# Performance work log

Hardware: AMD Instinct MI355X
Metric: run time of the kernel (lower is better)

Reference implementation:

```python
import jax, jax.numpy as jnp
import numpy as np

N_NODES = 100000
N_EDGES = 1600000
IN_FEATS = 16
H_FEAT = 128
NUM_CLASSES = 4
N_HIDDEN_LAYERS = 19  # layers 2..20 (128->128)
NEG_SLOPE = 0.01      # torch nn.LeakyReLU default


def setup_inputs() -> dict:
    key = jax.random.key(0)
    ks = jax.random.split(key, 10)
    node_feat = jax.random.normal(ks[0], (N_NODES, IN_FEATS), dtype=jnp.float32)
    edge_weight = jax.random.uniform(ks[1], (N_EDGES,), dtype=jnp.float32)
    src = jax.random.randint(ks[2], (N_EDGES,), 0, N_NODES, dtype=jnp.int32)
    dst = jax.random.randint(ks[3], (N_EDGES,), 0, N_NODES, dtype=jnp.int32)
    # Glorot-ish init for GraphConv weights, zero biases (DGL default)
    W1 = jax.random.normal(ks[4], (IN_FEATS, H_FEAT), dtype=jnp.float32) * (1.0 / np.sqrt(IN_FEATS))
    b1 = jnp.zeros((H_FEAT,), dtype=jnp.float32)
    W_stack = jax.random.normal(ks[5], (N_HIDDEN_LAYERS, H_FEAT, H_FEAT), dtype=jnp.float32) * (1.0 / np.sqrt(H_FEAT))
    b_stack = jnp.zeros((N_HIDDEN_LAYERS, H_FEAT), dtype=jnp.float32)
    fc_W = jax.random.normal(ks[6], (H_FEAT, NUM_CLASSES), dtype=jnp.float32) * (1.0 / np.sqrt(H_FEAT))
    fc_b = jnp.zeros((NUM_CLASSES,), dtype=jnp.float32)
    return {"node_feat": node_feat, "edge_weight": edge_weight, "src": src, "dst": dst,
            "W1": W1, "b1": b1, "W_stack": W_stack, "b_stack": b_stack,
            "fc_W": fc_W, "fc_b": fc_b}


def _degree_norms(src, dst, n_nodes, dtype):
    ones = jnp.ones(src.shape, dtype=dtype)
    out_deg = jax.ops.segment_sum(ones, src, num_segments=n_nodes)
    in_deg = jax.ops.segment_sum(ones, dst, num_segments=n_nodes)
    # DGL clamps degrees to min 1 for norm='both'
    inv_sqrt_out = jax.lax.rsqrt(jnp.maximum(out_deg, 1.0))
    inv_sqrt_in = jax.lax.rsqrt(jnp.maximum(in_deg, 1.0))
    return inv_sqrt_out, inv_sqrt_in


def _graph_conv(h, W, b, src, dst, ew, inv_sqrt_out, inv_sqrt_in, n_nodes):
    # DGL GraphConv norm='both' with edge_weight: u_mul_e message, sum at dst
    hs = h * inv_sqrt_out[:, None]                     # [N, F] src-side norm
    m = hs[src] * ew[:, None]                          # [E, F] edge messages
    agg = jax.ops.segment_sum(m, dst, num_segments=n_nodes)  # [N, F]
    agg = agg * inv_sqrt_in[:, None]                   # dst-side norm
    return agg @ W + b


def reference(node_feat, edge_weight, src, dst, W1, b1, W_stack, b_stack, fc_W, fc_b):
    n_nodes = node_feat.shape[0]
    iso, isi = _degree_norms(src, dst, n_nodes, node_feat.dtype)
    leaky = lambda x: jnp.where(x >= 0, x, NEG_SLOPE * x)

    h = leaky(_graph_conv(node_feat, W1, b1, src, dst, edge_weight, iso, isi, n_nodes))

    def body(h, wb):
        W, b = wb
        h = leaky(_graph_conv(h, W, b, src, dst, edge_weight, iso, isi, n_nodes))
        return h, None

    h, _ = jax.lax.scan(body, h, (W_stack, b_stack))
    return h @ fc_W + fc_b
```

## Files before the change

kernel.cpp:

```cpp
#include <hip/hip_runtime.h>

#define NN 100000
#define NE 1600000
#define HF 128
#define INF 16
#define NLAYERS 19

static inline int idiv(int a, int b) { return (a + b - 1) / b; }

__device__ __forceinline__ float leaky(float v) { return (v >= 0.f) ? v : 0.01f * v; }


__global__ __launch_bounds__(256) void k_deg1(const int* __restrict__ idx, int* __restrict__ deg, int e) {
  int i = (blockIdx.x * 256 + threadIdx.x) * 4;
  if (i + 4 <= e) {
    int4 v = *reinterpret_cast<const int4*>(idx + i);
    atomicAdd(&deg[v.x], 1);
    atomicAdd(&deg[v.y], 1);
    atomicAdd(&deg[v.z], 1);
    atomicAdd(&deg[v.w], 1);
  } else {
    for (; i < e; ++i) atomicAdd(&deg[idx[i]], 1);
  }
}

__global__ __launch_bounds__(256) void k_norms(const int* __restrict__ dout, const int* __restrict__ din,
                                               float* __restrict__ iso, float* __restrict__ isi, int n) {
  int i = blockIdx.x * 256 + threadIdx.x;
  if (i < n) {
    iso[i] = rsqrtf((float)(dout[i] > 1 ? dout[i] : 1));
    isi[i] = rsqrtf((float)(din[i] > 1 ? din[i] : 1));
  }
}

__global__ __launch_bounds__(1024) void k_scan(const int* __restrict__ cnt, int* __restrict__ rp, int n) {
  __shared__ int wsum[16];
  const int tid = threadIdx.x;
  const int lane = tid & 63;
  const int wid = tid >> 6;
  int carry = 0;
  for (int base = 0; base < n; base += 1024) {
    int i = base + tid;
    int v = (i < n) ? cnt[i] : 0;
    int x = v;
#pragma unroll
    for (int off = 1; off < 64; off <<= 1) {
      int t = __shfl_up(x, off, 64);
      if (lane >= off) x += t;
    }
    if (lane == 63) wsum[wid] = x;
    __syncthreads();
    if (wid == 0) {
      int s = (lane < 16) ? wsum[lane] : 0;
#pragma unroll
      for (int off = 1; off < 16; off <<= 1) {
        int t = __shfl_up(s, off, 64);
        if (lane >= off) s += t;
      }
      if (lane < 16) wsum[lane] = s;
    }
    __syncthreads();
    int woff = (wid > 0) ? wsum[wid - 1] : 0;
    if (i < n) rp[i] = carry + woff + x - v;
    carry += wsum[15];
    __syncthreads();
  }
  if (tid == 0) rp[n] = carry;
}

__global__ __launch_bounds__(256) void k_build(const int* __restrict__ src, const int* __restrict__ dst,
                                               const float* __restrict__ ew, const float* __restrict__ iso,
                                               const float* __restrict__ isi, const int* __restrict__ rp,
                                               int* __restrict__ cursor, int2* __restrict__ cv, int e) {
  int i = blockIdx.x * 256 + threadIdx.x;
  if (i < e) {
    int s = src[i], d = dst[i];
    int pos = rp[d] + atomicAdd(&cursor[d], 1);
    float v = ew[i] * iso[s] * isi[d];
    cv[pos] = make_int2(s, __float_as_int(v));
  }
}


__global__ __launch_bounds__(256) void k_spmm16(const float* __restrict__ x, const int* __restrict__ rp,
                                                const int2* __restrict__ cv, float* __restrict__ agg16, int n) {
  int t = blockIdx.x * 256 + threadIdx.x;
  int node = t >> 4, f = t & 15;
  if (node >= n) return;
  int e = rp[node], end = rp[node + 1];
  float a = 0.f;
  for (; e + 4 <= end; e += 4) {
    int2 q0 = cv[e], q1 = cv[e + 1], q2 = cv[e + 2], q3 = cv[e + 3];
    float x0 = x[(size_t)q0.x * INF + f];
    float x1 = x[(size_t)q1.x * INF + f];
    float x2 = x[(size_t)q2.x * INF + f];
    float x3 = x[(size_t)q3.x * INF + f];
    a = fmaf(__int_as_float(q0.y), x0, a);
    a = fmaf(__int_as_float(q1.y), x1, a);
    a = fmaf(__int_as_float(q2.y), x2, a);
    a = fmaf(__int_as_float(q3.y), x3, a);
  }
  for (; e < end; ++e) {
    int2 q = cv[e];
    a = fmaf(__int_as_float(q.y), x[(size_t)q.x * INF + f], a);
  }
  agg16[(size_t)node * INF + f] = a;
}

__global__ __launch_bounds__(256) void k_gemm16(const float* __restrict__ agg16, const float* __restrict__ W1,
                                                const float* __restrict__ b1, float* __restrict__ h, int n) {
  __shared__ float W1s[INF * HF];
  int tid = threadIdx.x;
  {
    float4* d4 = reinterpret_cast<float4*>(W1s);
    const float4* s4 = reinterpret_cast<const float4*>(W1);
    d4[tid] = s4[tid];
    d4[tid + 256] = s4[tid + 256];
  }
  __syncthreads();
  int t = blockIdx.x * 256 + tid;
  int node = t >> 7, c = t & 127;
  if (node >= n) return;
  const float* ar = agg16 + (size_t)node * INF;
  float4 a0 = *reinterpret_cast<const float4*>(ar);
  float4 a1 = *reinterpret_cast<const float4*>(ar + 4);
  float4 a2 = *reinterpret_cast<const float4*>(ar + 8);
  float4 a3 = *reinterpret_cast<const float4*>(ar + 12);
  float av[16] = {a0.x, a0.y, a0.z, a0.w, a1.x, a1.y, a1.z, a1.w,
                  a2.x, a2.y, a2.z, a2.w, a3.x, a3.y, a3.z, a3.w};
  float a = b1[c];
#pragma unroll
  for (int f = 0; f < INF; ++f) a = fmaf(av[f], W1s[f * HF + c], a);
  h[(size_t)t] = leaky(a);
}


__global__ __launch_bounds__(256) void k_spmm(const float* __restrict__ h, const int* __restrict__ rp,
                                              const int2* __restrict__ cv, float* __restrict__ agg, int n) {
  const int lane = threadIdx.x & 63;
  const int node = __builtin_amdgcn_readfirstlane(blockIdx.x * 4 + (threadIdx.x >> 6));
  if (node >= n) return;
  const int beg = rp[node], end = rp[node + 1];
  const size_t fo = (size_t)(lane << 1);
  float ax = 0.f, ay = 0.f;
  int e = beg;
  for (; e + 8 <= end; e += 8) {
    int2 q0 = cv[e + 0], q1 = cv[e + 1], q2 = cv[e + 2], q3 = cv[e + 3];
    int2 q4 = cv[e + 4], q5 = cv[e + 5], q6 = cv[e + 6], q7 = cv[e + 7];
    float2 x0 = *reinterpret_cast<const float2*>(h + (size_t)q0.x * HF + fo);
    float2 x1 = *reinterpret_cast<const float2*>(h + (size_t)q1.x * HF + fo);
    float2 x2 = *reinterpret_cast<const float2*>(h + (size_t)q2.x * HF + fo);
    float2 x3 = *reinterpret_cast<const float2*>(h + (size_t)q3.x * HF + fo);
    float2 x4 = *reinterpret_cast<const float2*>(h + (size_t)q4.x * HF + fo);
    float2 x5 = *reinterpret_cast<const float2*>(h + (size_t)q5.x * HF + fo);
    float2 x6 = *reinterpret_cast<const float2*>(h + (size_t)q6.x * HF + fo);
    float2 x7 = *reinterpret_cast<const float2*>(h + (size_t)q7.x * HF + fo);
    ax = fmaf(__int_as_float(q0.y), x0.x, ax); ay = fmaf(__int_as_float(q0.y), x0.y, ay);
    ax = fmaf(__int_as_float(q1.y), x1.x, ax); ay = fmaf(__int_as_float(q1.y), x1.y, ay);
    ax = fmaf(__int_as_float(q2.y), x2.x, ax); ay = fmaf(__int_as_float(q2.y), x2.y, ay);
    ax = fmaf(__int_as_float(q3.y), x3.x, ax); ay = fmaf(__int_as_float(q3.y), x3.y, ay);
    ax = fmaf(__int_as_float(q4.y), x4.x, ax); ay = fmaf(__int_as_float(q4.y), x4.y, ay);
    ax = fmaf(__int_as_float(q5.y), x5.x, ax); ay = fmaf(__int_as_float(q5.y), x5.y, ay);
    ax = fmaf(__int_as_float(q6.y), x6.x, ax); ay = fmaf(__int_as_float(q6.y), x6.y, ay);
    ax = fmaf(__int_as_float(q7.y), x7.x, ax); ay = fmaf(__int_as_float(q7.y), x7.y, ay);
  }
  if (e + 4 <= end) {
    int2 q0 = cv[e + 0], q1 = cv[e + 1], q2 = cv[e + 2], q3 = cv[e + 3];
    float2 x0 = *reinterpret_cast<const float2*>(h + (size_t)q0.x * HF + fo);
    float2 x1 = *reinterpret_cast<const float2*>(h + (size_t)q1.x * HF + fo);
    float2 x2 = *reinterpret_cast<const float2*>(h + (size_t)q2.x * HF + fo);
    float2 x3 = *reinterpret_cast<const float2*>(h + (size_t)q3.x * HF + fo);
    ax = fmaf(__int_as_float(q0.y), x0.x, ax); ay = fmaf(__int_as_float(q0.y), x0.y, ay);
    ax = fmaf(__int_as_float(q1.y), x1.x, ax); ay = fmaf(__int_as_float(q1.y), x1.y, ay);
    ax = fmaf(__int_as_float(q2.y), x2.x, ax); ay = fmaf(__int_as_float(q2.y), x2.y, ay);
    ax = fmaf(__int_as_float(q3.y), x3.x, ax); ay = fmaf(__int_as_float(q3.y), x3.y, ay);
    e += 4;
  }
  if (e + 2 <= end) {
    int2 q0 = cv[e + 0], q1 = cv[e + 1];
    float2 x0 = *reinterpret_cast<const float2*>(h + (size_t)q0.x * HF + fo);
    float2 x1 = *reinterpret_cast<const float2*>(h + (size_t)q1.x * HF + fo);
    ax = fmaf(__int_as_float(q0.y), x0.x, ax); ay = fmaf(__int_as_float(q0.y), x0.y, ay);
    ax = fmaf(__int_as_float(q1.y), x1.x, ax); ay = fmaf(__int_as_float(q1.y), x1.y, ay);
    e += 2;
  }
  if (e < end) {
    int2 q0 = cv[e];
    float2 x0 = *reinterpret_cast<const float2*>(h + (size_t)q0.x * HF + fo);
    ax = fmaf(__int_as_float(q0.y), x0.x, ax); ay = fmaf(__int_as_float(q0.y), x0.y, ay);
  }
  *reinterpret_cast<float2*>(agg + (size_t)node * HF + fo) = make_float2(ax, ay);
}

__global__ __launch_bounds__(256) void k_gemm(const float* __restrict__ A, const float* __restrict__ W,
                                              const float* __restrict__ bias, float* __restrict__ out, int n) {
  __shared__ float As[32][132];
  __shared__ float Ws[32][HF];
  const int tid = threadIdx.x;
  const int n0 = blockIdx.x * 128;
  const int ty = tid >> 4;
  const int tx = tid & 15;
  float acc[8][8];
#pragma unroll
  for (int i = 0; i < 8; i++)
#pragma unroll
    for (int j = 0; j < 8; j++) acc[i][j] = 0.f;

  for (int kc = 0; kc < HF; kc += 32) {
    {
      int kq = (tid & 7) * 4;
      int nl = tid >> 3;
#pragma unroll
      for (int p = 0; p < 4; ++p) {
        int nn = nl + p * 32;
        int ng = n0 + nn;
        float4 v = make_float4(0.f, 0.f, 0.f, 0.f);
        if (ng < n) v = *reinterpret_cast<const float4*>(A + (size_t)ng * HF + kc + kq);
        As[kq + 0][nn] = v.x;
        As[kq + 1][nn] = v.y;
        As[kq + 2][nn] = v.z;
        As[kq + 3][nn] = v.w;
      }
    }
    {
      int c4 = (tid & 31) * 4;
      int r = tid >> 5;
#pragma unroll
      for (int p = 0; p < 4; ++p) {
        int rr = r + p * 8;
        *reinterpret_cast<float4*>(&Ws[rr][c4]) =
            *reinterpret_cast<const float4*>(W + (size_t)(kc + rr) * HF + c4);
      }
    }
    __syncthreads();
#pragma unroll
    for (int k = 0; k < 32; ++k) {
      float4 a0 = *reinterpret_cast<const float4*>(&As[k][ty * 8]);
      float4 a1 = *reinterpret_cast<const float4*>(&As[k][ty * 8 + 4]);
      float4 w0 = *reinterpret_cast<const float4*>(&Ws[k][tx * 8]);
      float4 w1 = *reinterpret_cast<const float4*>(&Ws[k][tx * 8 + 4]);
      float a[8] = {a0.x, a0.y, a0.z, a0.w, a1.x, a1.y, a1.z, a1.w};
      float w[8] = {w0.x, w0.y, w0.z, w0.w, w1.x, w1.y, w1.z, w1.w};
#pragma unroll
      for (int i = 0; i < 8; i++)
#pragma unroll
        for (int j = 0; j < 8; j++) acc[i][j] = fmaf(a[i], w[j], acc[i][j]);
    }
    __syncthreads();
  }
  float bb[8];
#pragma unroll
  for (int j = 0; j < 8; j++) bb[j] = bias[tx * 8 + j];
#pragma unroll
  for (int i = 0; i < 8; i++) {
    int ng = n0 + ty * 8 + i;
    if (ng < n) {
      float o[8];
#pragma unroll
      for (int j = 0; j < 8; j++) o[j] = leaky(acc[i][j] + bb[j]);
      float4* dst4 = reinterpret_cast<float4*>(out + (size_t)ng * HF + tx * 8);
      dst4[0] = make_float4(o[0], o[1], o[2], o[3]);
      dst4[1] = make_float4(o[4], o[5], o[6], o[7]);
    }
  }
}


__global__ __launch_bounds__(256) void k_head(const float* __restrict__ h, const float* __restrict__ fcW,
                                              const float* __restrict__ fcb, float* __restrict__ out, int n) {
  int gw = (blockIdx.x * 256 + threadIdx.x) >> 6;
  int lane = threadIdx.x & 63;
  int node = gw * 8 + (lane >> 3);
  int part = lane & 7;
  float a0 = 0.f, a1 = 0.f, a2 = 0.f, a3 = 0.f;
  if (node < n) {
    const float* hp = h + (size_t)node * HF + part * 16;
#pragma unroll
    for (int i = 0; i < 16; i++) {
      float xv = hp[i];
      float4 wk = *reinterpret_cast<const float4*>(fcW + (part * 16 + i) * 4);
      a0 = fmaf(xv, wk.x, a0);
      a1 = fmaf(xv, wk.y, a1);
      a2 = fmaf(xv, wk.z, a2);
      a3 = fmaf(xv, wk.w, a3);
    }
  }
#pragma unroll
  for (int m = 1; m < 8; m <<= 1) {
    a0 += __shfl_xor(a0, m, 64);
    a1 += __shfl_xor(a1, m, 64);
    a2 += __shfl_xor(a2, m, 64);
    a3 += __shfl_xor(a3, m, 64);
  }
  if (part == 0 && node < n) {
    float4 o = make_float4(a0 + fcb[0], a1 + fcb[1], a2 + fcb[2], a3 + fcb[3]);
    *reinterpret_cast<float4*>(out + (size_t)node * 4) = o;
  }
}


extern "C" void kernel_launch(void* const* d_in, const int* in_sizes, int n_in,
                              void* d_out, int out_size, void* d_ws, size_t ws_size,
                              hipStream_t stream) {
  const float* x = (const float*)d_in[0];
  const float* ew = (const float*)d_in[1];
  const int* src = (const int*)d_in[2];
  const int* dst = (const int*)d_in[3];
  const float* W1 = (const float*)d_in[4];
  const float* b1 = (const float*)d_in[5];
  const float* Wst = (const float*)d_in[6];
  const float* bst = (const float*)d_in[7];
  const float* fcW = (const float*)d_in[8];
  const float* fcb = (const float*)d_in[9];
  float* out = (float*)d_out;

  const int n = NN, e = NE;
  char* w = (char*)d_ws;
  size_t off = 0;
  auto alloc = [&](size_t bytes) {
    void* p = w + off;
    off += (bytes + 511) & ~(size_t)511;
    return p;
  };
  int* dout = (int*)alloc((size_t)n * 4);
  int* din = (int*)alloc((size_t)n * 4);
  float* iso = (float*)alloc((size_t)n * 4);
  float* isi = (float*)alloc((size_t)n * 4);
  int* rp = (int*)alloc((size_t)(n + 1) * 4);
  int* cursor = (int*)alloc((size_t)n * 4);
  int2* cv = (int2*)alloc((size_t)e * 8);
  float* h = (float*)alloc((size_t)n * HF * 4);
  float* agg = (float*)alloc((size_t)n * HF * 4);
  float* agg16 = agg;

  hipMemsetAsync(dout, 0, (size_t)n * 4, stream);
  hipMemsetAsync(din, 0, (size_t)n * 4, stream);
  hipMemsetAsync(cursor, 0, (size_t)n * 4, stream);

  k_deg1<<<idiv(e, 1024), 256, 0, stream>>>(src, dout, e);
  k_deg1<<<idiv(e, 1024), 256, 0, stream>>>(dst, din, e);
  k_norms<<<idiv(n, 256), 256, 0, stream>>>(dout, din, iso, isi, n);
  k_scan<<<1, 1024, 0, stream>>>(din, rp, n);
  k_build<<<idiv(e, 256), 256, 0, stream>>>(src, dst, ew, iso, isi, rp, cursor, cv, e);

  k_spmm16<<<idiv(n * INF, 256), 256, 0, stream>>>(x, rp, cv, agg16, n);
  k_gemm16<<<idiv(n * HF, 256), 256, 0, stream>>>(agg16, W1, b1, h, n);

  for (int l = 0; l < NLAYERS; ++l) {
    k_spmm<<<idiv(n, 4), 256, 0, stream>>>(h, rp, cv, agg, n);
    k_gemm<<<idiv(n, 128), 256, 0, stream>>>(agg, Wst + (size_t)l * HF * HF, bst + (size_t)l * HF, h, n);
  }
  k_head<<<idiv(n * 8, 256), 256, 0, stream>>>(h, fcW, fcb, out, n);
}
```

Before: 3.702 ms.

## Fuse SpMM aggregation and dense GEMM into one per-layer kernel with ping-pong buffers

Replaces the separate spmm and gemm kernels with one fused kernel. Each block aggregates 64 nodes into shared memory (16 nodes per wave, processed one after another), then multiplies the tile by W and writes the leaky output to a second h buffer. This drops the global write and re-read of the intermediate agg array and one launch per layer. In exchange, each wave handles its nodes serially and the block holds a large shared tile, which lowers occupancy and the gather parallelism per block. The GEMM tile also shrinks from 128 to 64 rows and reads A as scalars.

```diff
diff --git a/kernel.cpp b/kernel.cpp
--- a/kernel.cpp
+++ b/kernel.cpp
@@ -135,93 +135,83 @@
 }
 
 
-__global__ __launch_bounds__(256) void k_spmm(const float* __restrict__ h, const int* __restrict__ rp,
-                                              const int2* __restrict__ cv, float* __restrict__ agg, int n) {
-  const int lane = threadIdx.x & 63;
-  const int node = __builtin_amdgcn_readfirstlane(blockIdx.x * 4 + (threadIdx.x >> 6));
-  if (node >= n) return;
-  const int beg = rp[node], end = rp[node + 1];
+__global__ __launch_bounds__(256) void k_fused(const float* __restrict__ hin, const int* __restrict__ rp,
+                                               const int2* __restrict__ cv, const float* __restrict__ W,
+                                               const float* __restrict__ bias, float* __restrict__ hout, int n) {
+  __shared__ float As[64][130];
+  __shared__ float Ws[32][132];
+  const int tid = threadIdx.x;
+  const int lane = tid & 63;
+  const int wv = tid >> 6;
+  const int n0 = blockIdx.x * 64;
   const size_t fo = (size_t)(lane << 1);
-  float ax = 0.f, ay = 0.f;
-  int e = beg;
-  for (; e + 8 <= end; e += 8) {
-    int2 q0 = cv[e + 0], q1 = cv[e + 1], q2 = cv[e + 2], q3 = cv[e + 3];
-    int2 q4 = cv[e + 4], q5 = cv[e + 5], q6 = cv[e + 6], q7 = cv[e + 7];
-    float2 x0 = *reinterpret_cast<const float2*>(h + (size_t)q0.x * HF + fo);
-    float2 x1 = *reinterpret_cast<const float2*>(h + (size_t)q1.x * HF + fo);
-    float2 x2 = *reinterpret_cast<const float2*>(h + (size_t)q2.x * HF + fo);
-    float2 x3 = *reinterpret_cast<const float2*>(h + (size_t)q3.x * HF + fo);
-    float2 x4 = *reinterpret_cast<const float2*>(h + (size_t)q4.x * HF + fo);
-    float2 x5 = *reinterpret_cast<const float2*>(h + (size_t)q5.x * HF + fo);
-    float2 x6 = *reinterpret_cast<const float2*>(h + (size_t)q6.x * HF + fo);
-    float2 x7 = *reinterpret_cast<const float2*>(h + (size_t)q7.x * HF + fo);
-    ax = fmaf(__int_as_float(q0.y), x0.x, ax); ay = fmaf(__int_as_float(q0.y), x0.y, ay);
-    ax = fmaf(__int_as_float(q1.y), x1.x, ax); ay = fmaf(__int_as_float(q1.y), x1.y, ay);
-    ax = fmaf(__int_as_float(q2.y), x2.x, ax); ay = fmaf(__int_as_float(q2.y), x2.y, ay);
-    ax = fmaf(__int_as_float(q3.y), x3.x, ax); ay = fmaf(__int_as_float(q3.y), x3.y, ay);
-    ax = fmaf(__int_as_float(q4.y), x4.x, ax); ay = fmaf(__int_as_float(q4.y), x4.y, ay);
-    ax = fmaf(__int_as_float(q5.y), x5.x, ax); ay = fmaf(__int_as_float(q5.y), x5.y, ay);
-    ax = fmaf(__int_as_float(q6.y), x6.x, ax); ay = fmaf(__int_as_float(q6.y), x6.y, ay);
-    ax = fmaf(__int_as_float(q7.y), x7.x, ax); ay = fmaf(__int_as_float(q7.y), x7.y, ay);
-  }
-  if (e + 4 <= end) {
-    int2 q0 = cv[e + 0], q1 = cv[e + 1], q2 = cv[e + 2], q3 = cv[e + 3];
-    float2 x0 = *reinterpret_cast<const float2*>(h + (size_t)q0.x * HF + fo);
-    float2 x1 = *reinterpret_cast<const float2*>(h + (size_t)q1.x * HF + fo);
-    float2 x2 = *reinterpret_cast<const float2*>(h + (size_t)q2.x * HF + fo);
-    float2 x3 = *reinterpret_cast<const float2*>(h + (size_t)q3.x * HF + fo);
-    ax = fmaf(__int_as_float(q0.y), x0.x, ax); ay = fmaf(__int_as_float(q0.y), x0.y, ay);
-    ax = fmaf(__int_as_float(q1.y), x1.x, ax); ay = fmaf(__int_as_float(q1.y), x1.y, ay);
-    ax = fmaf(__int_as_float(q2.y), x2.x, ax); ay = fmaf(__int_as_float(q2.y), x2.y, ay);
-    ax = fmaf(__int_as_float(q3.y), x3.x, ax); ay = fmaf(__int_as_float(q3.y), x3.y, ay);
-    e += 4;
-  }
-  if (e + 2 <= end) {
-    int2 q0 = cv[e + 0], q1 = cv[e + 1];
-    float2 x0 = *reinterpret_cast<const float2*>(h + (size_t)q0.x * HF + fo);
-    float2 x1 = *reinterpret_cast<const float2*>(h + (size_t)q1.x * HF + fo);
-    ax = fmaf(__int_as_float(q0.y), x0.x, ax); ay = fmaf(__int_as_float(q0.y), x0.y, ay);
-    ax = fmaf(__int_as_float(q1.y), x1.x, ax); ay = fmaf(__int_as_float(q1.y), x1.y, ay);
-    e += 2;
-  }
-  if (e < end) {
-    int2 q0 = cv[e];
-    float2 x0 = *reinterpret_cast<const float2*>(h + (size_t)q0.x * HF + fo);
-    ax = fmaf(__int_as_float(q0.y), x0.x, ax); ay = fmaf(__int_as_float(q0.y), x0.y, ay);
-  }
-  *reinterpret_cast<float2*>(agg + (size_t)node * HF + fo) = make_float2(ax, ay);
-}
-
-__global__ __launch_bounds__(256) void k_gemm(const float* __restrict__ A, const float* __restrict__ W,
-                                              const float* __restrict__ bias, float* __restrict__ out, int n) {
-  __shared__ float As[32][132];
-  __shared__ float Ws[32][HF];
-  const int tid = threadIdx.x;
-  const int n0 = blockIdx.x * 128;
+
+  for (int i = 0; i < 16; ++i) {
+    const int nl = wv * 16 + i;
+    const int node = n0 + nl;
+    float ax = 0.f, ay = 0.f;
+    if (node < n) {
+      int e = rp[node];
+      const int end = rp[node + 1];
+      for (; e + 8 <= end; e += 8) {
+        int2 q0 = cv[e + 0], q1 = cv[e + 1], q2 = cv[e + 2], q3 = cv[e + 3];
+        int2 q4 = cv[e + 4], q5 = cv[e + 5], q6 = cv[e + 6], q7 = cv[e + 7];
+        float2 x0 = *reinterpret_cast<const float2*>(hin + (size_t)q0.x * HF + fo);
+        float2 x1 = *reinterpret_cast<const float2*>(hin + (size_t)q1.x * HF + fo);
+        float2 x2 = *reinterpret_cast<const float2*>(hin + (size_t)q2.x * HF + fo);
+        float2 x3 = *reinterpret_cast<const float2*>(hin + (size_t)q3.x * HF + fo);
+        float2 x4 = *reinterpret_cast<const float2*>(hin + (size_t)q4.x * HF + fo);
+        float2 x5 = *reinterpret_cast<const float2*>(hin + (size_t)q5.x * HF + fo);
+        float2 x6 = *reinterpret_cast<const float2*>(hin + (size_t)q6.x * HF + fo);
+        float2 x7 = *reinterpret_cast<const float2*>(hin + (size_t)q7.x * HF + fo);
+        ax = fmaf(__int_as_float(q0.y), x0.x, ax); ay = fmaf(__int_as_float(q0.y), x0.y, ay);
+        ax = fmaf(__int_as_float(q1.y), x1.x, ax); ay = fmaf(__int_as_float(q1.y), x1.y, ay);
+        ax = fmaf(__int_as_float(q2.y), x2.x, ax); ay = fmaf(__int_as_float(q2.y), x2.y, ay);
+        ax = fmaf(__int_as_float(q3.y), x3.x, ax); ay = fmaf(__int_as_float(q3.y), x3.y, ay);
+        ax = fmaf(__int_as_float(q4.y), x4.x, ax); ay = fmaf(__int_as_float(q4.y), x4.y, ay);
+        ax = fmaf(__int_as_float(q5.y), x5.x, ax); ay = fmaf(__int_as_float(q5.y), x5.y, ay);
+        ax = fmaf(__int_as_float(q6.y), x6.x, ax); ay = fmaf(__int_as_float(q6.y), x6.y, ay);
+        ax = fmaf(__int_as_float(q7.y), x7.x, ax); ay = fmaf(__int_as_float(q7.y), x7.y, ay);
+      }
+      if (e + 4 <= end) {
+        int2 q0 = cv[e + 0], q1 = cv[e + 1], q2 = cv[e + 2], q3 = cv[e + 3];
+        float2 x0 = *reinterpret_cast<const float2*>(hin + (size_t)q0.x * HF + fo);
+        float2 x1 = *reinterpret_cast<const float2*>(hin + (size_t)q1.x * HF + fo);
+        float2 x2 = *reinterpret_cast<const float2*>(hin + (size_t)q2.x * HF + fo);
+        float2 x3 = *reinterpret_cast<const float2*>(hin + (size_t)q3.x * HF + fo);
+        ax = fmaf(__int_as_float(q0.y), x0.x, ax); ay = fmaf(__int_as_float(q0.y), x0.y, ay);
+        ax = fmaf(__int_as_float(q1.y), x1.x, ax); ay = fmaf(__int_as_float(q1.y), x1.y, ay);
+        ax = fmaf(__int_as_float(q2.y), x2.x, ax); ay = fmaf(__int_as_float(q2.y), x2.y, ay);
+        ax = fmaf(__int_as_float(q3.y), x3.x, ax); ay = fmaf(__int_as_float(q3.y), x3.y, ay);
+        e += 4;
+      }
+      if (e + 2 <= end) {
+        int2 q0 = cv[e + 0], q1 = cv[e + 1];
+        float2 x0 = *reinterpret_cast<const float2*>(hin + (size_t)q0.x * HF + fo);
+        float2 x1 = *reinterpret_cast<const float2*>(hin + (size_t)q1.x * HF + fo);
+        ax = fmaf(__int_as_float(q0.y), x0.x, ax); ay = fmaf(__int_as_float(q0.y), x0.y, ay);
+        ax = fmaf(__int_as_float(q1.y), x1.x, ax); ay = fmaf(__int_as_float(q1.y), x1.y, ay);
+        e += 2;
+      }
+      if (e < end) {
+        int2 q0 = cv[e];
+        float2 x0 = *reinterpret_cast<const float2*>(hin + (size_t)q0.x * HF + fo);
+        ax = fmaf(__int_as_float(q0.y), x0.x, ax); ay = fmaf(__int_as_float(q0.y), x0.y, ay);
+      }
+    }
+    *reinterpret_cast<float2*>(&As[nl][lane << 1]) = make_float2(ax, ay);
+  }
+  __syncthreads();
+
   const int ty = tid >> 4;
   const int tx = tid & 15;
-  float acc[8][8];
-#pragma unroll
-  for (int i = 0; i < 8; i++)
+  float acc[4][8];
+#pragma unroll
+  for (int i = 0; i < 4; i++)
 #pragma unroll
     for (int j = 0; j < 8; j++) acc[i][j] = 0.f;
 
   for (int kc = 0; kc < HF; kc += 32) {
-    {
-      int kq = (tid & 7) * 4;
-      int nl = tid >> 3;
-#pragma unroll
-      for (int p = 0; p < 4; ++p) {
-        int nn = nl + p * 32;
-        int ng = n0 + nn;
-        float4 v = make_float4(0.f, 0.f, 0.f, 0.f);
-        if (ng < n) v = *reinterpret_cast<const float4*>(A + (size_t)ng * HF + kc + kq);
-        As[kq + 0][nn] = v.x;
-        As[kq + 1][nn] = v.y;
-        As[kq + 2][nn] = v.z;
-        As[kq + 3][nn] = v.w;
-      }
-    }
     {
       int c4 = (tid & 31) * 4;
       int r = tid >> 5;
@@ -235,16 +225,18 @@
     __syncthreads();
 #pragma unroll
     for (int k = 0; k < 32; ++k) {
-      float4 a0 = *reinterpret_cast<const float4*>(&As[k][ty * 8]);
-      float4 a1 = *reinterpret_cast<const float4*>(&As[k][ty * 8 + 4]);
+      float a0 = As[ty * 4 + 0][kc + k];
+      float a1 = As[ty * 4 + 1][kc + k];
+      float a2 = As[ty * 4 + 2][kc + k];
+      float a3 = As[ty * 4 + 3][kc + k];
       float4 w0 = *reinterpret_cast<const float4*>(&Ws[k][tx * 8]);
       float4 w1 = *reinterpret_cast<const float4*>(&Ws[k][tx * 8 + 4]);
-      float a[8] = {a0.x, a0.y, a0.z, a0.w, a1.x, a1.y, a1.z, a1.w};
-      float w[8] = {w0.x, w0.y, w0.z, w0.w, w1.x, w1.y, w1.z, w1.w};
-#pragma unroll
-      for (int i = 0; i < 8; i++)
-#pragma unroll
-        for (int j = 0; j < 8; j++) acc[i][j] = fmaf(a[i], w[j], acc[i][j]);
+      float wv8[8] = {w0.x, w0.y, w0.z, w0.w, w1.x, w1.y, w1.z, w1.w};
+      float av[4] = {a0, a1, a2, a3};
+#pragma unroll
+      for (int i = 0; i < 4; i++)
+#pragma unroll
+        for (int j = 0; j < 8; j++) acc[i][j] = fmaf(av[i], wv8[j], acc[i][j]);
     }
     __syncthreads();
   }
@@ -252,13 +244,13 @@
 #pragma unroll
   for (int j = 0; j < 8; j++) bb[j] = bias[tx * 8 + j];
 #pragma unroll
-  for (int i = 0; i < 8; i++) {
-    int ng = n0 + ty * 8 + i;
-    if (ng < n) {
+  for (int i = 0; i < 4; i++) {
+    int node = n0 + ty * 4 + i;
+    if (node < n) {
       float o[8];
 #pragma unroll
       for (int j = 0; j < 8; j++) o[j] = leaky(acc[i][j] + bb[j]);
-      float4* dst4 = reinterpret_cast<float4*>(out + (size_t)ng * HF + tx * 8);
+      float4* dst4 = reinterpret_cast<float4*>(hout + (size_t)node * HF + tx * 8);
       dst4[0] = make_float4(o[0], o[1], o[2], o[3]);
       dst4[1] = make_float4(o[4], o[5], o[6], o[7]);
     }
@@ -329,9 +321,9 @@
   int* rp = (int*)alloc((size_t)(n + 1) * 4);
   int* cursor = (int*)alloc((size_t)n * 4);
   int2* cv = (int2*)alloc((size_t)e * 8);
-  float* h = (float*)alloc((size_t)n * HF * 4);
-  float* agg = (float*)alloc((size_t)n * HF * 4);
-  float* agg16 = agg;
+  float* h0 = (float*)alloc((size_t)n * HF * 4);
+  float* h1 = (float*)alloc((size_t)n * HF * 4);
+  float* agg16 = h1;
 
   hipMemsetAsync(dout, 0, (size_t)n * 4, stream);
   hipMemsetAsync(din, 0, (size_t)n * 4, stream);
@@ -344,11 +336,13 @@
   k_build<<<idiv(e, 256), 256, 0, stream>>>(src, dst, ew, iso, isi, rp, cursor, cv, e);
 
   k_spmm16<<<idiv(n * INF, 256), 256, 0, stream>>>(x, rp, cv, agg16, n);
-  k_gemm16<<<idiv(n * HF, 256), 256, 0, stream>>>(agg16, W1, b1, h, n);
-
+  k_gemm16<<<idiv(n * HF, 256), 256, 0, stream>>>(agg16, W1, b1, h0, n);
+
+  float* ha = h0;
+  float* hb = h1;
   for (int l = 0; l < NLAYERS; ++l) {
-    k_spmm<<<idiv(n, 4), 256, 0, stream>>>(h, rp, cv, agg, n);
-    k_gemm<<<idiv(n, 128), 256, 0, stream>>>(agg, Wst + (size_t)l * HF * HF, bst + (size_t)l * HF, h, n);
-  }
-  k_head<<<idiv(n * 8, 256), 256, 0, stream>>>(h, fcW, fcb, out, n);
-}
+    k_fused<<<idiv(n, 64), 256, 0, stream>>>(ha, rp, cv, Wst + (size_t)l * HF * HF, bst + (size_t)l * HF, hb, n);
+    float* t = ha; ha = hb; hb = t;
+  }
+  k_head<<<idiv(n * 8, 256), 256, 0, stream>>>(ha, fcW, fcb, out, n);
+}
```

Result: slower. 4.501 ms (+21.6%).

## Double-buffer GEMM shared tiles with register prefetch and conflict-free split layout

Applied to the files above, without the earlier changes.

Rewrites the dense 128x128 GEMM to double-buffer the A and W tiles in shared memory, prefetching the next K-chunk into registers while the current chunk is computed. This needs one barrier per chunk instead of two. It also remaps each thread's 8x8 outputs into two 4-wide groups 64 apart to cut LDS bank conflicts, and changes the A load pattern so consecutive threads handle consecutive nodes. The cost is twice the shared memory and more live registers, which may lower occupancy. The GEMM is likely a minor share of runtime next to the gather aggregation.

```diff
diff --git a/kernel.cpp b/kernel.cpp
--- a/kernel.cpp
+++ b/kernel.cpp
@@ -194,73 +194,111 @@
 
 __global__ __launch_bounds__(256) void k_gemm(const float* __restrict__ A, const float* __restrict__ W,
                                               const float* __restrict__ bias, float* __restrict__ out, int n) {
-  __shared__ float As[32][132];
-  __shared__ float Ws[32][HF];
+  __shared__ float As[2][32][132];
+  __shared__ float Ws[2][32][132];
   const int tid = threadIdx.x;
   const int n0 = blockIdx.x * 128;
   const int ty = tid >> 4;
   const int tx = tid & 15;
+
+  const int anode = tid & 127;
+  const int akq_base = ((tid >> 7) & 1) * 4;
+  const int wr = tid >> 3;
+  const int wc16 = (tid & 7) * 16;
+
+  float4 aReg[4], wReg[4];
+
+#pragma unroll
+  for (int it = 0; it < 4; ++it) {
+    int ng = n0 + anode;
+    int k = akq_base + it * 8;
+    aReg[it] = (ng < n) ? *reinterpret_cast<const float4*>(A + (size_t)ng * HF + k)
+                        : make_float4(0.f, 0.f, 0.f, 0.f);
+  }
+#pragma unroll
+  for (int p = 0; p < 4; ++p)
+    wReg[p] = *reinterpret_cast<const float4*>(W + (size_t)wr * HF + wc16 + p * 4);
+
+#pragma unroll
+  for (int it = 0; it < 4; ++it) {
+    int k = akq_base + it * 8;
+    As[0][k + 0][anode] = aReg[it].x;
+    As[0][k + 1][anode] = aReg[it].y;
+    As[0][k + 2][anode] = aReg[it].z;
+    As[0][k + 3][anode] = aReg[it].w;
+  }
+#pragma unroll
+  for (int p = 0; p < 4; ++p)
+    *reinterpret_cast<float4*>(&Ws[0][wr][wc16 + p * 4]) = wReg[p];
+  __syncthreads();
+
   float acc[8][8];
 #pragma unroll
   for (int i = 0; i < 8; i++)
 #pragma unroll
     for (int j = 0; j < 8; j++) acc[i][j] = 0.f;
 
-  for (int kc = 0; kc < HF; kc += 32) {
-    {
-      int kq = (tid & 7) * 4;
-      int nl = tid >> 3;
-#pragma unroll
-      for (int p = 0; p < 4; ++p) {
-        int nn = nl + p * 32;
-        int ng = n0 + nn;
-        float4 v = make_float4(0.f, 0.f, 0.f, 0.f);
-        if (ng < n) v = *reinterpret_cast<const float4*>(A + (size_t)ng * HF + kc + kq);
-        As[kq + 0][nn] = v.x;
-        As[kq + 1][nn] = v.y;
-        As[kq + 2][nn] = v.z;
-        As[kq + 3][nn] = v.w;
+  for (int c = 0; c < 4; ++c) {
+    const int b = c & 1;
+    if (c < 3) {
+      const int kc = (c + 1) * 32;
+#pragma unroll
+      for (int it = 0; it < 4; ++it) {
+        int ng = n0 + anode;
+        int k = kc + akq_base + it * 8;
+        aReg[it] = (ng < n) ? *reinterpret_cast<const float4*>(A + (size_t)ng * HF + k)
+                            : make_float4(0.f, 0.f, 0.f, 0.f);
       }
-    }
-    {
-      int c4 = (tid & 31) * 4;
-      int r = tid >> 5;
-#pragma unroll
-      for (int p = 0; p < 4; ++p) {
-        int rr = r + p * 8;
-        *reinterpret_cast<float4*>(&Ws[rr][c4]) =
-            *reinterpret_cast<const float4*>(W + (size_t)(kc + rr) * HF + c4);
+#pragma unroll
+      for (int p = 0; p < 4; ++p)
+        wReg[p] = *reinterpret_cast<const float4*>(W + (size_t)(kc + wr) * HF + wc16 + p * 4);
+    }
+#pragma unroll
+    for (int k = 0; k < 32; ++k) {
+      float4 a0 = *reinterpret_cast<const float4*>(&As[b][k][ty * 4]);
+      float4 a1 = *reinterpret_cast<const float4*>(&As[b][k][ty * 4 + 64]);
+      float4 w0 = *reinterpret_cast<const float4*>(&Ws[b][k][tx * 4]);
+      float4 w1 = *reinterpret_cast<const float4*>(&Ws[b][k][tx * 4 + 64]);
+      float av[8] = {a0.x, a0.y, a0.z, a0.w, a1.x, a1.y, a1.z, a1.w};
+      float wv[8] = {w0.x, w0.y, w0.z, w0.w, w1.x, w1.y, w1.z, w1.w};
+#pragma unroll
+      for (int i = 0; i < 8; i++)
+#pragma unroll
+        for (int j = 0; j < 8; j++) acc[i][j] = fmaf(av[i], wv[j], acc[i][j]);
+    }
+    if (c < 3) {
+      const int nb = b ^ 1;
+#pragma unroll
+      for (int it = 0; it < 4; ++it) {
+        int k = akq_base + it * 8;
+        As[nb][k + 0][anode] = aReg[it].x;
+        As[nb][k + 1][anode] = aReg[it].y;
+        As[nb][k + 2][anode] = aReg[it].z;
+        As[nb][k + 3][anode] = aReg[it].w;
       }
+#pragma unroll
+      for (int p = 0; p < 4; ++p)
+        *reinterpret_cast<float4*>(&Ws[nb][wr][wc16 + p * 4]) = wReg[p];
     }
     __syncthreads();
-#pragma unroll
-    for (int k = 0; k < 32; ++k) {
-      float4 a0 = *reinterpret_cast<const float4*>(&As[k][ty * 8]);
-      float4 a1 = *reinterpret_cast<const float4*>(&As[k][ty * 8 + 4]);
-      float4 w0 = *reinterpret_cast<const float4*>(&Ws[k][tx * 8]);
-      float4 w1 = *reinterpret_cast<const float4*>(&Ws[k][tx * 8 + 4]);
-      float a[8] = {a0.x, a0.y, a0.z, a0.w, a1.x, a1.y, a1.z, a1.w};
-      float w[8] = {w0.x, w0.y, w0.z, w0.w, w1.x, w1.y, w1.z, w1.w};
-#pragma unroll
-      for (int i = 0; i < 8; i++)
-#pragma unroll
-        for (int j = 0; j < 8; j++) acc[i][j] = fmaf(a[i], w[j], acc[i][j]);
-    }
-    __syncthreads();
-  }
-  float bb[8];
-#pragma unroll
-  for (int j = 0; j < 8; j++) bb[j] = bias[tx * 8 + j];
-#pragma unroll
-  for (int i = 0; i < 8; i++) {
-    int ng = n0 + ty * 8 + i;
-    if (ng < n) {
-      float o[8];
-#pragma unroll
-      for (int j = 0; j < 8; j++) o[j] = leaky(acc[i][j] + bb[j]);
-      float4* dst4 = reinterpret_cast<float4*>(out + (size_t)ng * HF + tx * 8);
-      dst4[0] = make_float4(o[0], o[1], o[2], o[3]);
-      dst4[1] = make_float4(o[4], o[5], o[6], o[7]);
+  }
+
+  float4 bb0 = *reinterpret_cast<const float4*>(bias + tx * 4);
+  float4 bb1 = *reinterpret_cast<const float4*>(bias + tx * 4 + 64);
+  float bb[8] = {bb0.x, bb0.y, bb0.z, bb0.w, bb1.x, bb1.y, bb1.z, bb1.w};
+#pragma unroll
+  for (int g = 0; g < 2; ++g) {
+#pragma unroll
+    for (int i = 0; i < 4; ++i) {
+      int node = n0 + ty * 4 + g * 64 + i;
+      if (node < n) {
+        int ai = g * 4 + i;
+        float o[8];
+#pragma unroll
+        for (int j = 0; j < 8; j++) o[j] = leaky(acc[ai][j] + bb[j]);
+        *reinterpret_cast<float4*>(out + (size_t)node * HF + tx * 4) = make_float4(o[0], o[1], o[2], o[3]);
+        *reinterpret_cast<float4*>(out + (size_t)node * HF + tx * 4 + 64) = make_float4(o[4], o[5], o[6], o[7]);
+      }
     }
   }
 }
```

Measured after the change: 6.020 ms. 1.63x slower.
